# Optimization experiments

Hardware: AMD Instinct MI355X
Metric: run time of the kernel (lower is better)

The kernel has to match this reference:

```python
import jax, jax.numpy as jnp
import numpy as np

T = 8192
D_IN = 512
D_QK = 64
D_V = 64


def setup_inputs() -> dict:
    key = jax.random.key(0)
    kx, kq, kk, kv, kl = jax.random.split(key, 5)
    x = jax.random.normal(kx, (T, D_IN), dtype=jnp.float32)
    Wq = jax.random.normal(kq, (D_IN, D_QK), dtype=jnp.float32) * 0.02
    Wk = jax.random.normal(kk, (D_IN, D_QK), dtype=jnp.float32) * 0.02
    Wv = jax.random.normal(kv, (D_IN, D_V), dtype=jnp.float32) * 0.02
    l = jax.random.normal(kl, (T, T), dtype=jnp.float32) * 0.02
    return {"x": x, "Wq": Wq, "Wk": Wk, "Wv": Wv, "l": l}


def reference(x, Wq, Wk, Wv, l):
    # q: [T, d_qk], k: [T, d_qk], v: [T, d_v]
    q = x @ Wq
    k = x @ Wk
    v = x @ Wv
    # scores: [T, S] = (q k^T) elementwise-weighted by learned tril matrix
    scores = jnp.einsum("tn,sn->ts", q, k) * jnp.tril(l)
    # output: [T, d_v]
    return scores @ v
```

## Files before the change

kernel.cpp:

```cpp
#include <hip/hip_runtime.h>
#include <hip/hip_bf16.h>

#define TT 8192
#define DIN 512
#define DQK 64

typedef __attribute__((ext_vector_type(8))) short short8;
typedef __attribute__((ext_vector_type(4))) float f32x4;

__global__ __launch_bounds__(256) void zero_kernel(float* __restrict__ out, int n4)
{
    int i = blockIdx.x * 256 + threadIdx.x;
    if (i < n4) ((f32x4*)out)[i] = (f32x4){0.f, 0.f, 0.f, 0.f};
}

__global__ __launch_bounds__(256) void wconv_kernel(
    const float* __restrict__ Wq, const float* __restrict__ Wk, const float* __restrict__ Wv,
    __hip_bfloat16* __restrict__ wtb)
{
    __shared__ float tile[64][65];
    const int m = blockIdx.y;
    const float* W = m == 0 ? Wq : (m == 1 ? Wk : Wv);
    const int k0 = blockIdx.x * 64;
    const int tid = threadIdx.x;

    {
        const int col4 = (tid & 15) * 4;
        #pragma unroll
        for (int it = 0; it < 4; ++it) {
            const int row = (tid >> 4) + it * 16;
            float4 v = *(const float4*)&W[(size_t)(k0 + row) * DQK + col4];
            tile[row][col4 + 0] = v.x; tile[row][col4 + 1] = v.y;
            tile[row][col4 + 2] = v.z; tile[row][col4 + 3] = v.w;
        }
    }
    __syncthreads();
    {
        const int d = tid >> 2;
        const int kc = (tid & 3) * 16;
        short tmp[16];
        #pragma unroll
        for (int j = 0; j < 16; ++j) {
            __hip_bfloat16 h = __float2bfloat16(tile[kc + j][d]);
            tmp[j] = *(short*)&h;
        }
        short* dst = (short*)wtb + ((size_t)m * 64 + d) * DIN + k0 + kc;
        *(short8*)dst       = *(short8*)&tmp[0];
        *(short8*)(dst + 8) = *(short8*)&tmp[8];
    }
}

#define PP 72

__global__ __launch_bounds__(256) void proj_kernel(
    const float* __restrict__ x,
    const __hip_bfloat16* __restrict__ wtb,
    __hip_bfloat16* __restrict__ qb, __hip_bfloat16* __restrict__ kb,
    __hip_bfloat16* __restrict__ vt)
{
    __shared__ short xb[64][PP];
    __shared__ short wb[3][64][PP];

    const int rowBase = blockIdx.x * 64;
    const int tid = threadIdx.x;
    const int lane = tid & 63;
    const int w = tid >> 6;
    const int lo = lane & 15, hi = lane >> 4;

    f32x4 acc[3][4];
    #pragma unroll
    for (int m = 0; m < 3; ++m)
        #pragma unroll
        for (int cf = 0; cf < 4; ++cf) acc[m][cf] = (f32x4){0.f, 0.f, 0.f, 0.f};

    for (int kk = 0; kk < DIN; kk += 64) {
        {
            const int r = tid >> 2;
            const int c0 = (tid & 3) * 16;
            const float* xp = x + (size_t)(rowBase + r) * DIN + kk + c0;
            short tmp[16];
            #pragma unroll
            for (int j = 0; j < 16; j += 4) {
                float4 v = *(const float4*)(xp + j);
                __hip_bfloat16 h0 = __float2bfloat16(v.x);
                __hip_bfloat16 h1 = __float2bfloat16(v.y);
                __hip_bfloat16 h2 = __float2bfloat16(v.z);
                __hip_bfloat16 h3 = __float2bfloat16(v.w);
                tmp[j + 0] = *(short*)&h0; tmp[j + 1] = *(short*)&h1;
                tmp[j + 2] = *(short*)&h2; tmp[j + 3] = *(short*)&h3;
            }
            *(short8*)&xb[r][c0]     = *(short8*)&tmp[0];
            *(short8*)&xb[r][c0 + 8] = *(short8*)&tmp[8];
        }
        {
            const int d = tid >> 2;
            const int kc = (tid & 3) * 16;
            #pragma unroll
            for (int m = 0; m < 3; ++m) {
                const short* src = (const short*)wtb + ((size_t)m * 64 + d) * DIN + kk + kc;
                *(short8*)&wb[m][d][kc]     = *(const short8*)src;
                *(short8*)&wb[m][d][kc + 8] = *(const short8*)(src + 8);
            }
        }
        __syncthreads();

        short8 a0 = *(short8*)&xb[w * 16 + lo][hi * 8];
        short8 a1 = *(short8*)&xb[w * 16 + lo][32 + hi * 8];
        #pragma unroll
        for (int m = 0; m < 3; ++m) {
            #pragma unroll
            for (int cf = 0; cf < 4; ++cf) {
                short8 b0 = *(short8*)&wb[m][cf * 16 + lo][hi * 8];
                short8 b1 = *(short8*)&wb[m][cf * 16 + lo][32 + hi * 8];
                acc[m][cf] = __builtin_amdgcn_mfma_f32_16x16x32_bf16(a0, b0, acc[m][cf], 0, 0, 0);
                acc[m][cf] = __builtin_amdgcn_mfma_f32_16x16x32_bf16(a1, b1, acc[m][cf], 0, 0, 0);
            }
        }
        __syncthreads();
    }

    #pragma unroll
    for (int cf = 0; cf < 4; ++cf) {
        #pragma unroll
        for (int r = 0; r < 4; ++r) {
            const int tg = rowBase + w * 16 + hi * 4 + r;
            const int d  = cf * 16 + lo;
            __hip_bfloat16 hq = __float2bfloat16(acc[0][cf][r]);
            __hip_bfloat16 hk = __float2bfloat16(acc[1][cf][r]);
            __hip_bfloat16 hv = __float2bfloat16(acc[2][cf][r]);
            qb[(size_t)tg * DQK + d] = hq;
            kb[(size_t)tg * DQK + d] = hk;
            vt[(size_t)d * TT + tg]  = hv;
        }
    }
}

#define TM 128
#define TS 64
#define SCHUNK 256
#define LP 72

__global__ __launch_bounds__(512) void attn_kernel(
    const __hip_bfloat16* __restrict__ qb,
    const __hip_bfloat16* __restrict__ kb,
    const __hip_bfloat16* __restrict__ vt,
    const float* __restrict__ l,
    float* __restrict__ out)
{
    __shared__ short K_lds[TS][LP];
    __shared__ short V_lds[DQK][LP];
    __shared__ short S_lds[8][16][LP];

    const int t0 = blockIdx.x * TM;
    const int sStart = blockIdx.y * SCHUNK;
    if (sStart >= t0 + TM) return;
    const int sEnd = min(sStart + SCHUNK, t0 + TM);

    const int tid = threadIdx.x;
    const int lane = tid & 63;
    const int w = tid >> 6;
    const int lo = lane & 15, hi = lane >> 4;
    const int trow = t0 + w * 16;

    short8 qf0, qf1;
    {
        const short* qp = (const short*)qb + (size_t)(trow + lo) * DQK;
        qf0 = *(const short8*)(qp + hi * 8);
        qf1 = *(const short8*)(qp + 32 + hi * 8);
    }

    f32x4 acc_o[4];
    #pragma unroll
    for (int i = 0; i < 4; ++i) acc_o[i] = (f32x4){0.f, 0.f, 0.f, 0.f};

    float lvC[4][4];
    float lvN[4][4] = {{0.f}};
    {
        #pragma unroll
        for (int sub = 0; sub < 4; ++sub) {
            const int s_glob = sStart + sub * 16 + lo;
            #pragma unroll
            for (int r = 0; r < 4; ++r) {
                const int tg = trow + hi * 4 + r;
                lvC[sub][r] = (s_glob <= tg) ? l[(size_t)tg * TT + s_glob] : 0.f;
            }
        }
    }

    for (int s0 = sStart; s0 < sEnd; s0 += TS) {
        {
            const int row = tid >> 3;
            const int c8 = (tid & 7) * 8;
            *(short8*)&K_lds[row][c8] =
                *(const short8*)((const short*)kb + (size_t)(s0 + row) * DQK + c8);
            *(short8*)&V_lds[row][c8] =
                *(const short8*)((const short*)vt + (size_t)row * TT + s0 + c8);
        }
        __syncthreads();

        const bool active = (s0 <= trow + 15);
        const int sN = s0 + TS;
        const bool act_next = (sN < sEnd) && (sN <= trow + 15);

        if (act_next) {
            #pragma unroll
            for (int sub = 0; sub < 4; ++sub) {
                const int s_glob = sN + sub * 16 + lo;
                #pragma unroll
                for (int r = 0; r < 4; ++r) {
                    const int tg = trow + hi * 4 + r;
                    lvN[sub][r] = (s_glob <= tg) ? l[(size_t)tg * TT + s_glob] : 0.f;
                }
            }
        }

        if (active) {
            #pragma unroll
            for (int sub = 0; sub < 4; ++sub) {
                f32x4 acc = (f32x4){0.f, 0.f, 0.f, 0.f};
                short8 b0 = *(short8*)&K_lds[sub * 16 + lo][hi * 8];
                short8 b1 = *(short8*)&K_lds[sub * 16 + lo][32 + hi * 8];
                acc = __builtin_amdgcn_mfma_f32_16x16x32_bf16(qf0, b0, acc, 0, 0, 0);
                acc = __builtin_amdgcn_mfma_f32_16x16x32_bf16(qf1, b1, acc, 0, 0, 0);
                #pragma unroll
                for (int r = 0; r < 4; ++r) {
                    float sv = acc[r] * lvC[sub][r];
                    __hip_bfloat16 h = __float2bfloat16(sv);
                    S_lds[w][hi * 4 + r][sub * 16 + lo] = *(short*)&h;
                }
            }
            short8 a0 = *(short8*)&S_lds[w][lo][hi * 8];
            short8 a1 = *(short8*)&S_lds[w][lo][32 + hi * 8];
            #pragma unroll
            for (int ds = 0; ds < 4; ++ds) {
                short8 b0 = *(short8*)&V_lds[ds * 16 + lo][hi * 8];
                short8 b1 = *(short8*)&V_lds[ds * 16 + lo][32 + hi * 8];
                acc_o[ds] = __builtin_amdgcn_mfma_f32_16x16x32_bf16(a0, b0, acc_o[ds], 0, 0, 0);
                acc_o[ds] = __builtin_amdgcn_mfma_f32_16x16x32_bf16(a1, b1, acc_o[ds], 0, 0, 0);
            }
        }
        __syncthreads();

        #pragma unroll
        for (int sub = 0; sub < 4; ++sub)
            #pragma unroll
            for (int r = 0; r < 4; ++r)
                lvC[sub][r] = lvN[sub][r];
    }

    #pragma unroll
    for (int ds = 0; ds < 4; ++ds) {
        #pragma unroll
        for (int r = 0; r < 4; ++r) {
            const int tg = trow + hi * 4 + r;
            atomicAdd(&out[(size_t)tg * DQK + ds * 16 + lo], acc_o[ds][r]);
        }
    }
}

extern "C" void kernel_launch(void* const* d_in, const int* in_sizes, int n_in,
                              void* d_out, int out_size, void* d_ws, size_t ws_size,
                              hipStream_t stream) {
    const float* x  = (const float*)d_in[0];
    const float* Wq = (const float*)d_in[1];
    const float* Wk = (const float*)d_in[2];
    const float* Wv = (const float*)d_in[3];
    const float* l  = (const float*)d_in[4];
    float* out = (float*)d_out;

    __hip_bfloat16* qb  = (__hip_bfloat16*)d_ws;
    __hip_bfloat16* kb  = qb + (size_t)TT * DQK;
    __hip_bfloat16* vt  = kb + (size_t)TT * DQK;
    __hip_bfloat16* wtb = vt + (size_t)TT * DQK;

    zero_kernel<<<(out_size / 4 + 255) / 256, 256, 0, stream>>>(out, out_size / 4);
    wconv_kernel<<<dim3(DIN / 64, 3), 256, 0, stream>>>(Wq, Wk, Wv, wtb);
    proj_kernel<<<TT / 64, 256, 0, stream>>>(x, wtb, qb, kb, vt);
    attn_kernel<<<dim3(TT / TM, TT / SCHUNK), 512, 0, stream>>>(qb, kb, vt, l, out);
}
```

Before: 72.57 us.

## Drop shared K/V staging; load MFMA operands directly from global per wave

```diff
diff --git a/kernel.cpp b/kernel.cpp
--- a/kernel.cpp
+++ b/kernel.cpp
@@ -138,7 +138,6 @@
 #define TM 128
 #define TS 64
 #define SCHUNK 256
-#define LP 72
 
 __global__ __launch_bounds__(512) void attn_kernel(
     const __hip_bfloat16* __restrict__ qb,
@@ -147,9 +146,7 @@
     const float* __restrict__ l,
     float* __restrict__ out)
 {
-    __shared__ short K_lds[TS][LP];
-    __shared__ short V_lds[DQK][LP];
-    __shared__ short S_lds[8][16][LP];
+    __shared__ short S_lds[8][16][72];
 
     const int t0 = blockIdx.x * TM;
     const int sStart = blockIdx.y * SCHUNK;
@@ -162,6 +159,9 @@
     const int lo = lane & 15, hi = lane >> 4;
     const int trow = t0 + w * 16;
 
+    const int myEnd = min(sEnd, trow + 16);
+    if (myEnd <= sStart) return;
+
     short8 qf0, qf1;
     {
         const short* qp = (const short*)qb + (size_t)(trow + lo) * DQK;
@@ -173,73 +173,61 @@
     #pragma unroll
     for (int i = 0; i < 4; ++i) acc_o[i] = (f32x4){0.f, 0.f, 0.f, 0.f};
 
+    const int r0 = hi * 4;
+
     float lvC[4][4];
-    float lvN[4][4] = {{0.f}};
-    {
+    float lvN[4][4];
+    #pragma unroll
+    for (int sub = 0; sub < 4; ++sub) {
+        const int s_glob = sStart + sub * 16 + lo;
+        #pragma unroll
+        for (int r = 0; r < 4; ++r) {
+            const int tg = trow + r0 + r;
+            lvC[sub][r] = (s_glob <= tg) ? l[(size_t)tg * TT + s_glob] : 0.f;
+        }
+    }
+
+    for (int s0 = sStart; s0 < myEnd; s0 += TS) {
+        const int sN = s0 + TS;
+        const bool pf = (sN < myEnd);
+
         #pragma unroll
         for (int sub = 0; sub < 4; ++sub) {
-            const int s_glob = sStart + sub * 16 + lo;
+            const int s_glob = sN + sub * 16 + lo;
             #pragma unroll
             for (int r = 0; r < 4; ++r) {
-                const int tg = trow + hi * 4 + r;
-                lvC[sub][r] = (s_glob <= tg) ? l[(size_t)tg * TT + s_glob] : 0.f;
-            }
-        }
-    }
-
-    for (int s0 = sStart; s0 < sEnd; s0 += TS) {
-        {
-            const int row = tid >> 3;
-            const int c8 = (tid & 7) * 8;
-            *(short8*)&K_lds[row][c8] =
-                *(const short8*)((const short*)kb + (size_t)(s0 + row) * DQK + c8);
-            *(short8*)&V_lds[row][c8] =
-                *(const short8*)((const short*)vt + (size_t)row * TT + s0 + c8);
-        }
-        __syncthreads();
-
-        const bool active = (s0 <= trow + 15);
-        const int sN = s0 + TS;
-        const bool act_next = (sN < sEnd) && (sN <= trow + 15);
-
-        if (act_next) {
-            #pragma unroll
-            for (int sub = 0; sub < 4; ++sub) {
-                const int s_glob = sN + sub * 16 + lo;
-                #pragma unroll
-                for (int r = 0; r < 4; ++r) {
-                    const int tg = trow + hi * 4 + r;
-                    lvN[sub][r] = (s_glob <= tg) ? l[(size_t)tg * TT + s_glob] : 0.f;
-                }
-            }
-        }
-
-        if (active) {
-            #pragma unroll
-            for (int sub = 0; sub < 4; ++sub) {
-                f32x4 acc = (f32x4){0.f, 0.f, 0.f, 0.f};
-                short8 b0 = *(short8*)&K_lds[sub * 16 + lo][hi * 8];
-                short8 b1 = *(short8*)&K_lds[sub * 16 + lo][32 + hi * 8];
-                acc = __builtin_amdgcn_mfma_f32_16x16x32_bf16(qf0, b0, acc, 0, 0, 0);
-                acc = __builtin_amdgcn_mfma_f32_16x16x32_bf16(qf1, b1, acc, 0, 0, 0);
-                #pragma unroll
-                for (int r = 0; r < 4; ++r) {
-                    float sv = acc[r] * lvC[sub][r];
-                    __hip_bfloat16 h = __float2bfloat16(sv);
-                    S_lds[w][hi * 4 + r][sub * 16 + lo] = *(short*)&h;
-                }
-            }
-            short8 a0 = *(short8*)&S_lds[w][lo][hi * 8];
-            short8 a1 = *(short8*)&S_lds[w][lo][32 + hi * 8];
-            #pragma unroll
-            for (int ds = 0; ds < 4; ++ds) {
-                short8 b0 = *(short8*)&V_lds[ds * 16 + lo][hi * 8];
-                short8 b1 = *(short8*)&V_lds[ds * 16 + lo][32 + hi * 8];
-                acc_o[ds] = __builtin_amdgcn_mfma_f32_16x16x32_bf16(a0, b0, acc_o[ds], 0, 0, 0);
-                acc_o[ds] = __builtin_amdgcn_mfma_f32_16x16x32_bf16(a1, b1, acc_o[ds], 0, 0, 0);
-            }
-        }
-        __syncthreads();
+                const int tg = trow + r0 + r;
+                lvN[sub][r] = (pf && s_glob <= tg) ? l[(size_t)tg * TT + s_glob] : 0.f;
+            }
+        }
+
+        const short* kbase = (const short*)kb + (size_t)s0 * DQK;
+        #pragma unroll
+        for (int sub = 0; sub < 4; ++sub) {
+            const short* krow = kbase + (size_t)(sub * 16 + lo) * DQK;
+            short8 b0 = *(const short8*)(krow + hi * 8);
+            short8 b1 = *(const short8*)(krow + 32 + hi * 8);
+            f32x4 acc = (f32x4){0.f, 0.f, 0.f, 0.f};
+            acc = __builtin_amdgcn_mfma_f32_16x16x32_bf16(qf0, b0, acc, 0, 0, 0);
+            acc = __builtin_amdgcn_mfma_f32_16x16x32_bf16(qf1, b1, acc, 0, 0, 0);
+            #pragma unroll
+            for (int r = 0; r < 4; ++r) {
+                float sv = acc[r] * lvC[sub][r];
+                __hip_bfloat16 h = __float2bfloat16(sv);
+                S_lds[w][r0 + r][sub * 16 + lo] = *(short*)&h;
+            }
+        }
+
+        short8 a0 = *(short8*)&S_lds[w][lo][hi * 8];
+        short8 a1 = *(short8*)&S_lds[w][lo][32 + hi * 8];
+        #pragma unroll
+        for (int ds = 0; ds < 4; ++ds) {
+            const short* vrow = (const short*)vt + (size_t)(ds * 16 + lo) * TT + s0;
+            short8 b0 = *(const short8*)(vrow + hi * 8);
+            short8 b1 = *(const short8*)(vrow + 32 + hi * 8);
+            acc_o[ds] = __builtin_amdgcn_mfma_f32_16x16x32_bf16(a0, b0, acc_o[ds], 0, 0, 0);
+            acc_o[ds] = __builtin_amdgcn_mfma_f32_16x16x32_bf16(a1, b1, acc_o[ds], 0, 0, 0);
+        }
 
         #pragma unroll
         for (int sub = 0; sub < 4; ++sub)
@@ -252,7 +240,7 @@
     for (int ds = 0; ds < 4; ++ds) {
         #pragma unroll
         for (int r = 0; r < 4; ++r) {
-            const int tg = trow + hi * 4 + r;
+            const int tg = trow + r0 + r;
             atomicAdd(&out[(size_t)tg * DQK + ds * 16 + lo], acc_o[ds][r]);
         }
     }
```

Result: slower. 127.8 us (+76.1%).

## Retile attention to 64-row blocks with longer S chunks and nontemporal l loads

Applied to the files above, without the earlier changes.

```diff
diff --git a/kernel.cpp b/kernel.cpp
--- a/kernel.cpp
+++ b/kernel.cpp
@@ -135,12 +135,12 @@
     }
 }
 
-#define TM 128
+#define TM 64
 #define TS 64
-#define SCHUNK 256
+#define SCHUNK 512
 #define LP 72
 
-__global__ __launch_bounds__(512) void attn_kernel(
+__global__ __launch_bounds__(256) void attn_kernel(
     const __hip_bfloat16* __restrict__ qb,
     const __hip_bfloat16* __restrict__ kb,
     const __hip_bfloat16* __restrict__ vt,
@@ -149,7 +149,7 @@
 {
     __shared__ short K_lds[TS][LP];
     __shared__ short V_lds[DQK][LP];
-    __shared__ short S_lds[8][16][LP];
+    __shared__ short S_lds[4][16][LP];
 
     const int t0 = blockIdx.x * TM;
     const int sStart = blockIdx.y * SCHUNK;
@@ -161,6 +161,8 @@
     const int w = tid >> 6;
     const int lo = lane & 15, hi = lane >> 4;
     const int trow = t0 + w * 16;
+    const int r0 = hi * 4;
+    const bool waveActive = (sStart <= trow + 15);
 
     short8 qf0, qf1;
     {
@@ -174,27 +176,31 @@
     for (int i = 0; i < 4; ++i) acc_o[i] = (f32x4){0.f, 0.f, 0.f, 0.f};
 
     float lvC[4][4];
-    float lvN[4][4] = {{0.f}};
-    {
+    float lvN[4][4];
+    if (waveActive) {
         #pragma unroll
         for (int sub = 0; sub < 4; ++sub) {
             const int s_glob = sStart + sub * 16 + lo;
             #pragma unroll
             for (int r = 0; r < 4; ++r) {
-                const int tg = trow + hi * 4 + r;
-                lvC[sub][r] = (s_glob <= tg) ? l[(size_t)tg * TT + s_glob] : 0.f;
+                const int tg = trow + r0 + r;
+                lvC[sub][r] = (s_glob <= tg)
+                    ? __builtin_nontemporal_load(&l[(size_t)tg * TT + s_glob]) : 0.f;
             }
         }
     }
 
     for (int s0 = sStart; s0 < sEnd; s0 += TS) {
         {
-            const int row = tid >> 3;
             const int c8 = (tid & 7) * 8;
-            *(short8*)&K_lds[row][c8] =
-                *(const short8*)((const short*)kb + (size_t)(s0 + row) * DQK + c8);
-            *(short8*)&V_lds[row][c8] =
-                *(const short8*)((const short*)vt + (size_t)row * TT + s0 + c8);
+            #pragma unroll
+            for (int it = 0; it < 2; ++it) {
+                const int row = (tid >> 3) + it * 32;
+                *(short8*)&K_lds[row][c8] =
+                    *(const short8*)((const short*)kb + (size_t)(s0 + row) * DQK + c8);
+                *(short8*)&V_lds[row][c8] =
+                    *(const short8*)((const short*)vt + (size_t)row * TT + s0 + c8);
+            }
         }
         __syncthreads();
 
@@ -203,13 +209,25 @@
         const bool act_next = (sN < sEnd) && (sN <= trow + 15);
 
         if (act_next) {
-            #pragma unroll
-            for (int sub = 0; sub < 4; ++sub) {
-                const int s_glob = sN + sub * 16 + lo;
+            if (sN + 63 <= trow) {
                 #pragma unroll
-                for (int r = 0; r < 4; ++r) {
-                    const int tg = trow + hi * 4 + r;
-                    lvN[sub][r] = (s_glob <= tg) ? l[(size_t)tg * TT + s_glob] : 0.f;
+                for (int sub = 0; sub < 4; ++sub) {
+                    const int s_glob = sN + sub * 16 + lo;
+                    #pragma unroll
+                    for (int r = 0; r < 4; ++r)
+                        lvN[sub][r] = __builtin_nontemporal_load(
+                            &l[(size_t)(trow + r0 + r) * TT + s_glob]);
+                }
+            } else {
+                #pragma unroll
+                for (int sub = 0; sub < 4; ++sub) {
+                    const int s_glob = sN + sub * 16 + lo;
+                    #pragma unroll
+                    for (int r = 0; r < 4; ++r) {
+                        const int tg = trow + r0 + r;
+                        lvN[sub][r] = (s_glob <= tg)
+                            ? __builtin_nontemporal_load(&l[(size_t)tg * TT + s_glob]) : 0.f;
+                    }
                 }
             }
         }
@@ -226,7 +244,7 @@
                 for (int r = 0; r < 4; ++r) {
                     float sv = acc[r] * lvC[sub][r];
                     __hip_bfloat16 h = __float2bfloat16(sv);
-                    S_lds[w][hi * 4 + r][sub * 16 + lo] = *(short*)&h;
+                    S_lds[w][r0 + r][sub * 16 + lo] = *(short*)&h;
                 }
             }
             short8 a0 = *(short8*)&S_lds[w][lo][hi * 8];
@@ -248,12 +266,14 @@
                 lvC[sub][r] = lvN[sub][r];
     }
 
-    #pragma unroll
-    for (int ds = 0; ds < 4; ++ds) {
-        #pragma unroll
-        for (int r = 0; r < 4; ++r) {
-            const int tg = trow + hi * 4 + r;
-            atomicAdd(&out[(size_t)tg * DQK + ds * 16 + lo], acc_o[ds][r]);
+    if (waveActive) {
+        #pragma unroll
+        for (int ds = 0; ds < 4; ++ds) {
+            #pragma unroll
+            for (int r = 0; r < 4; ++r) {
+                const int tg = trow + r0 + r;
+                atomicAdd(&out[(size_t)tg * DQK + ds * 16 + lo], acc_o[ds][r]);
+            }
         }
     }
 }
@@ -276,5 +296,5 @@
     zero_kernel<<<(out_size / 4 + 255) / 256, 256, 0, stream>>>(out, out_size / 4);
     wconv_kernel<<<dim3(DIN / 64, 3), 256, 0, stream>>>(Wq, Wk, Wv, wtb);
     proj_kernel<<<TT / 64, 256, 0, stream>>>(x, wtb, qb, kb, vt);
-    attn_kernel<<<dim3(TT / TM, TT / SCHUNK), 512, 0, stream>>>(qb, kb, vt, l, out);
-}
+    attn_kernel<<<dim3(TT / TM, TT / SCHUNK), 256, 0, stream>>>(qb, kb, vt, l, out);
+}
```

After: 79.80 us. +10.0%, slower.
